# Performance work log

Measured on AMD Instinct MI355X. Metric: run time of the kernel, lower is better.

## Reference

```python
import jax, jax.numpy as jnp
import numpy as np

N = 50000      # nodes in the graph (len(vertices))
E = 800000     # edges per adjacency
D = 128        # n_feature (pretrained embedding dim)
V = 100000     # n_input (entity vocab)
OUT = 20       # n_output
L = 7          # n_hidden layers
BN_EPS = 1e-5


def setup_inputs() -> dict:
    key = jax.random.key(0)
    ks = jax.random.split(key, 12)
    s = 1.0 / np.sqrt(D)
    return {
        "vertices": jax.random.randint(ks[0], (N,), 0, V),
        "edge_index": jax.random.randint(ks[1], (L, 2, E), 0, N),
        "edge_weight": jax.random.uniform(ks[2], (L, E), jnp.float32),
        "emb_table": jax.random.normal(ks[3], (V, D), jnp.float32) * 0.02,
        "gcn_w_hidden": jax.random.normal(ks[4], (L - 1, D, D), jnp.float32) * s,
        "gcn_b_hidden": jnp.zeros((L - 1, D), jnp.float32),
        "gcn_w_out": jax.random.normal(ks[5], (D, OUT), jnp.float32) * s,
        "gcn_b_out": jnp.zeros((OUT,), jnp.float32),
        "bn_gamma_hidden": jnp.ones((L - 1, D), jnp.float32),
        "bn_beta_hidden": jnp.zeros((L - 1, D), jnp.float32),
        "bn_gamma_out": jnp.ones((OUT,), jnp.float32),
        "bn_beta_out": jnp.zeros((OUT,), jnp.float32),
        "te_wl": jax.random.normal(ks[6], (L - 1, D, D), jnp.float32) * s,
        "te_wc": jax.random.normal(ks[7], (L - 1, D, D), jnp.float32) * s,
        "te_b": jnp.zeros((L - 1, D), jnp.float32),
        "mask_w": jax.random.normal(ks[8], (V,), jnp.float32) * 0.02,
        "mask_b": jnp.zeros((OUT,), jnp.float32),
    }


def _spmm(src, dst, w, x):
    # out[i] = sum_{e: dst[e]==i} w[e] * x[src[e]]  (sparse adj @ x)
    return jax.ops.segment_sum(w[:, None] * x[src], dst, num_segments=N)


def _batchnorm(x, gamma, beta):
    # BatchNorm1d over the node (batch) axis, training-mode batch statistics
    m = x.mean(axis=0)
    v = x.var(axis=0)
    return (x - m) * jax.lax.rsqrt(v + BN_EPS) * gamma + beta


def reference(vertices, edge_index, edge_weight, emb_table,
              gcn_w_hidden, gcn_b_hidden, gcn_w_out, gcn_b_out,
              bn_gamma_hidden, bn_beta_hidden, bn_gamma_out, bn_beta_out,
              te_wl, te_wc, te_b, mask_w, mask_b):
    x = emb_table[vertices]                               # [N, D]
    for i in range(L):
        last_x = x
        if i < L - 1:
            support = x @ gcn_w_hidden[i]                 # [N, D]
            h = _spmm(edge_index[i, 0], edge_index[i, 1], edge_weight[i], support)
            h = h + gcn_b_hidden[i]
            h = _batchnorm(h, bn_gamma_hidden[i], bn_beta_hidden[i])
            h = jax.nn.relu(h)                            # dropout: eval mode (identity)
            j = (i - 1) % (L - 1)  # faithful to temporal_cells[i-1] (i=0 hits index -1)
            g = jax.nn.sigmoid(last_x @ te_wl[j] + h @ te_wc[j] + te_b[j])
            x = g * h + (1.0 - g) * last_x                # temporal gating cell
        else:
            support = x @ gcn_w_out                       # [N, OUT]
            h = _spmm(edge_index[i, 0], edge_index[i, 1], edge_weight[i], support)
            h = h + gcn_b_out
            x = _batchnorm(h, bn_gamma_out, bn_beta_out)
    x = jax.nn.relu(x)                                    # [N, OUT]
    out = jax.nn.sigmoid(mask_w[vertices] @ x + mask_b)   # MaskLinear + sigmoid -> [OUT]
    return out
```

## Files before the change

### kernel.cpp

```cpp
#include <hip/hip_runtime.h>
#include <hip/hip_fp16.h>

#define NN 50000
#define EE 800000
#define DIM 128
#define OUTC 20
#define LL 7
#define LE (LL*EE)
#define LN (LL*NN)
#define BN_EPS 1e-5f
#define LSTRIDE 136
#define NREP 64
#define NBUK 196
#define GMS  200
#define NBLK 200
#define CH   4000
#define CH4  (CH/4)
#define SCN  (LL*NBUK*NBLK)
#define FSCAP 4864
#define STATSZ (6*NREP*256 + 8*64 + 8*32 + 8)
#define STATSZ4 (STATSZ/4)

typedef __attribute__((ext_vector_type(8))) short short8;
typedef __attribute__((ext_vector_type(4))) float f32x4;

static __device__ __forceinline__ float sigm(float z){ return 1.0f/(1.0f+expf(-z)); }
static __device__ __forceinline__ unsigned short f2bf(float f){
  unsigned int u = __float_as_uint(f);
  u += 0x7FFF + ((u>>16)&1);
  return (unsigned short)(u>>16);
}
static __device__ __forceinline__ float bf2f(unsigned short s){
  return __uint_as_float(((unsigned int)s)<<16);
}

__global__ __launch_bounds__(256) void k_pre(const float* __restrict__ wh,
    const float* __restrict__ tewl, const float* __restrict__ tewc,
    const float* __restrict__ wout,
    unsigned short* __restrict__ Wt, unsigned short* __restrict__ WtO,
    const int* __restrict__ ei, int* __restrict__ Gm, float* __restrict__ stats){
  int bid = blockIdx.x;
  int t = threadIdx.x;
  if (bid < 1152){
    int gid = bid*256+t;
    int m = gid>>14; int idx = gid&16383;
    int n = idx>>7, k = idx&127;
    const float* src = (m<6)? wh + (size_t)m*16384
                     : (m<12)? tewl + (size_t)(m-6)*16384
                     : tewc + (size_t)(m-12)*16384;
    Wt[gid] = f2bf(src[k*128+n]);
  } else if (bid < 1168){
    int idx = (bid-1152)*256+t;
    int n = idx>>7, k = idx&127;
    WtO[idx] = (n<OUTC)? f2bf(wout[k*OUTC+n]) : (unsigned short)0;
  } else if (bid < 2568){
    int bb = bid-1168;
    int l = bb / NBLK, b = bb - l*NBLK;
    __shared__ int h[NBUK];
    if (t<NBUK) h[t]=0;
    const int4* dsts = (const int4*)(ei + (size_t)(2*l+1)*EE + b*CH);
    int4 dv[4];
    #pragma unroll
    for (int i=0;i<4;i++){
      int k4 = t + i*256;
      if (k4<CH4) dv[i] = dsts[k4];
    }
    __syncthreads();
    #pragma unroll
    for (int i=0;i<4;i++){
      int k4 = t + i*256;
      if (k4<CH4){
        atomicAdd(&h[dv[i].x>>8], 1);
        atomicAdd(&h[dv[i].y>>8], 1);
        atomicAdd(&h[dv[i].z>>8], 1);
        atomicAdd(&h[dv[i].w>>8], 1);
      }
    }
    __syncthreads();
    int* g = Gm + (size_t)(l*NBLK+b)*GMS;
    if (t<NBUK) g[t]=h[t];
  } else {
    int z = (bid-2568)*256+t;
    if (z < STATSZ4) ((float4*)stats)[z] = make_float4(0.f,0.f,0.f,0.f);
  }
}

__global__ __launch_bounds__(256) void k_scan1p(const int* __restrict__ Gm,
    int* __restrict__ part, int* __restrict__ bsums){
  __shared__ int s[256];
  int t = threadIdx.x;
  int base = blockIdx.x*4096 + t*16;
  int v[16]; int sum = 0;
  #pragma unroll
  for (int i=0;i<16;i++){
    int idx = base+i; int val = 0;
    if (idx < SCN){
      int l = idx/(NBUK*NBLK);
      int r = idx - l*(NBUK*NBLK);
      int buk = r/NBLK, b = r - buk*NBLK;
      val = Gm[(size_t)(l*NBLK+b)*GMS + buk];
    }
    v[i]=val; sum+=val;
  }
  s[t]=sum; __syncthreads();
  for (int off=1; off<256; off<<=1){
    int x = (t>=off)? s[t-off] : 0;
    __syncthreads(); s[t]+=x; __syncthreads();
  }
  if (t==255) bsums[blockIdx.x] = s[255];
  int run = s[t]-sum;
  #pragma unroll
  for (int i=0;i<16;i++){ if (base+i<SCN) part[base+i]=run; run += v[i]; }
}

__global__ __launch_bounds__(1024) void k_scan2(int* bsums, int nb){
  __shared__ int s[1024];
  int t=threadIdx.x;
  int v = (t<nb)? bsums[t]:0;
  s[t]=v; __syncthreads();
  for (int off=1; off<1024; off<<=1){
    int x=(t>=off)? s[t-off]:0; __syncthreads(); s[t]+=x; __syncthreads();
  }
  if (t<nb) bsums[t] = s[t]-v;
}

__global__ __launch_bounds__(256) void k_bscatter(const int* __restrict__ ei,
    const float* __restrict__ ew, const int* __restrict__ S,
    const int* __restrict__ bsums, const int* __restrict__ Gm,
    unsigned int* __restrict__ btmpP, unsigned char* __restrict__ btmpD){
  int l = blockIdx.x / NBLK, b = blockIdx.x - l*NBLK;
  int t = threadIdx.x;
  __shared__ int bstart[NBUK], cur[NBUK], runb[NBUK];
  __shared__ int wsum[4];
  __shared__ unsigned int  ebP[CH];
  __shared__ unsigned short ebM[CH];
  const int4*   srcs = (const int4*)(ei + (size_t)(2*l)*EE + b*CH);
  const int4*   dsts = (const int4*)(ei + (size_t)(2*l+1)*EE + b*CH);
  const float4* wsrc = (const float4*)(ew + (size_t)l*EE + b*CH);
  int4 sv[4], dv[4]; float4 wv[4];
  #pragma unroll
  for (int i=0;i<4;i++){
    int k4 = t + i*256;
    if (k4<CH4){
      sv[i] = srcs[k4];
      dv[i] = dsts[k4];
      wv[i] = wsrc[k4];
    }
  }
  int v = (t<NBUK)? Gm[(size_t)(l*NBLK+b)*GMS + t] : 0;
  int incl = v;
  #pragma unroll
  for (int d=1; d<64; d<<=1){
    int n = __shfl_up(incl, d, 64);
    if ((t&63) >= d) incl += n;
  }
  if ((t&63)==63) wsum[t>>6] = incl;
  __syncthreads();
  {
    int wv_ = t>>6, add = 0;
    if (wv_>0) add += wsum[0];
    if (wv_>1) add += wsum[1];
    if (wv_>2) add += wsum[2];
    incl += add;
  }
  if (t<NBUK){
    bstart[t]=incl-v; cur[t]=incl-v;
    int sidx = (l*NBUK+t)*NBLK + b;
    runb[t] = S[sidx] + bsums[sidx>>12];
  }
  __syncthreads();
  #define PUTE(SRC,DST,WF) { int buk=(DST)>>8; int pos=atomicAdd(&cur[buk],1); \
    unsigned short hw=__half_as_ushort(__float2half(WF)); \
    ebP[pos]=(unsigned)(SRC)|((unsigned)hw<<16); \
    ebM[pos]=(unsigned short)(((DST)&255)|(buk<<8)); }
  #pragma unroll
  for (int i=0;i<4;i++){
    int k4 = t + i*256;
    if (k4<CH4){
      PUTE(sv[i].x, dv[i].x, wv[i].x);
      PUTE(sv[i].y, dv[i].y, wv[i].y);
      PUTE(sv[i].z, dv[i].z, wv[i].z);
      PUTE(sv[i].w, dv[i].w, wv[i].w);
    }
  }
  #undef PUTE
  __syncthreads();
  for (int k=t;k<CH;k+=256){
    unsigned short m = ebM[k];
    int buk = m>>8;
    int gp = runb[buk] + (k - bstart[buk]);
    btmpP[gp] = ebP[k];
    btmpD[gp] = (unsigned char)(m&255);
  }
}

__global__ __launch_bounds__(256) void k_fsort(const unsigned int* __restrict__ btmpP,
    const unsigned char* __restrict__ btmpD, const int* __restrict__ S,
    const int* __restrict__ bsums,
    unsigned int* __restrict__ sedge, int* __restrict__ offs){
  int lbuk = blockIdx.x;
  int l = lbuk/NBUK, bl = lbuk - l*NBUK;
  int t = threadIdx.x;
  int i0 = lbuk*NBLK, i1 = i0+NBLK;
  int base = S[i0] + bsums[i0>>12];
  int end  = (i1==SCN)? LE : (S[i1] + bsums[i1>>12]);
  int nE = end - base;
  __shared__ int cnt[256];
  __shared__ int wsum[4];
  __shared__ unsigned int stg[FSCAP];
  cnt[t]=0;
  __syncthreads();
  for (int k=t; k<nE; k+=256) atomicAdd(&cnt[btmpD[base+k]], 1);
  __syncthreads();
  int c = cnt[t];
  int incl = c;
  #pragma unroll
  for (int d=1; d<64; d<<=1){
    int n = __shfl_up(incl, d, 64);
    if ((t&63) >= d) incl += n;
  }
  if ((t&63)==63) wsum[t>>6] = incl;
  __syncthreads();
  {
    int wv_ = t>>6, add = 0;
    if (wv_>0) add += wsum[0];
    if (wv_>1) add += wsum[1];
    if (wv_>2) add += wsum[2];
    incl += add;
  }
  int excl = incl - c;
  {
    int node = bl*256+t;
    if (node<NN) offs[(size_t)l*NN+node] = base + excl;
  }
  if (lbuk==0 && t==255) offs[LN]=LE;
  if (nE <= FSCAP){
    cnt[t] = excl;
    __syncthreads();
    for (int k=t; k<nE; k+=256){
      int d = btmpD[base+k];
      int r = atomicAdd(&cnt[d],1);
      stg[r] = btmpP[base+k];
    }
    __syncthreads();
    for (int k=t; k<nE; k+=256) sedge[base+k] = stg[k];
  } else {
    cnt[t] = base + excl;
    __syncthreads();
    for (int k=t; k<nE; k+=256){
      int d = btmpD[base+k];
      int r = atomicAdd(&cnt[d],1);
      sedge[r] = btmpP[base+k];
    }
  }
}

__global__ __launch_bounds__(256) void k_gemm_sup_emb(const int* __restrict__ verts,
    const float* __restrict__ emb, const unsigned short* __restrict__ Wt,
    unsigned short* __restrict__ Y, unsigned short* __restrict__ xout, int M){
  __shared__ unsigned short Xs[32*LSTRIDE];
  int tid = threadIdx.x;
  int row0 = blockIdx.x*32;
  #pragma unroll
  for (int it=0; it<2; it++){
    int idx = tid + it*256;
    int r = idx>>4, k8 = idx&15;
    short8 w = short8(0);
    if (row0+r < M){
      int v = verts[row0+r];
      const float4* p = (const float4*)emb + (size_t)v*32 + k8*2;
      float4 v0 = p[0], v1 = p[1];
      w[0]=(short)f2bf(v0.x); w[1]=(short)f2bf(v0.y); w[2]=(short)f2bf(v0.z); w[3]=(short)f2bf(v0.w);
      w[4]=(short)f2bf(v1.x); w[5]=(short)f2bf(v1.y); w[6]=(short)f2bf(v1.z); w[7]=(short)f2bf(v1.w);
      *(short8*)(xout + (size_t)(row0+r)*128 + k8*8) = w;
    }
    *(short8*)&Xs[r*LSTRIDE + k8*8] = w;
  }
  __syncthreads();
  int w = tid>>6, lane = tid&63, m = lane&15, q = lane>>4;
  int rw = (w&1)*16, cw = (w>>1)*64;
  f32x4 acc[4];
  #pragma unroll
  for (int nt=0;nt<4;nt++){ acc[nt][0]=0.f; acc[nt][1]=0.f; acc[nt][2]=0.f; acc[nt][3]=0.f; }
  #pragma unroll
  for (int kc=0; kc<4; kc++){
    short8 a = *(const short8*)&Xs[(rw+m)*LSTRIDE + kc*32 + 8*q];
    #pragma unroll
    for (int nt=0; nt<4; nt++){
      short8 b = *(const short8*)&Wt[(size_t)(cw+nt*16+m)*128 + kc*32 + 8*q];
      acc[nt] = __builtin_amdgcn_mfma_f32_16x16x32_bf16(a, b, acc[nt], 0,0,0);
    }
  }
  #pragma unroll
  for (int nt=0; nt<4; nt++){
    #pragma unroll
    for (int i=0;i<4;i++){
      int rr = row0 + rw + 4*q + i;
      if (rr<M) Y[(size_t)rr*128 + cw + nt*16 + m] = f2bf(acc[nt][i]);
    }
  }
}

template<int FUSE>
__global__ __launch_bounds__(256,4) void k_gemm_gate2(const unsigned short* __restrict__ H,
    const float* __restrict__ stL,
    const float* __restrict__ gamma, const float* __restrict__ beta,
    const unsigned short* __restrict__ Wl, const unsigned short* __restrict__ Wc,
    const unsigned short* __restrict__ Wn, const float* __restrict__ teb,
    unsigned short* __restrict__ x, unsigned short* __restrict__ supY, int M){
  __shared__ unsigned short XsX[64*LSTRIDE];
  __shared__ unsigned short XsH[64*LSTRIDE];
  __shared__ float sSt[256];
  int tid = threadIdx.x;
  int row0 = blockIdx.x*64;
  int k8 = tid&15;
  int w = tid>>6, lane = tid&63, m = lane&15, q = lane>>4;
  int cw = w*32;
  float4 g0 = *(const float4*)(gamma + k8*8), g1 = *(const float4*)(gamma + k8*8 + 4);
  float4 b0v = *(const float4*)(beta  + k8*8), b1v = *(const float4*)(beta  + k8*8 + 4);
  float tb0 = teb[cw+m], tb1 = teb[cw+16+m];
  short8 xv[4], hv[4];
  #pragma unroll
  for (int it=0; it<4; it++){
    int r = (tid + it*256)>>4;
    xv[it] = short8(0); hv[it] = short8(0);
    if (row0+r < M){
      xv[it] = *(const short8*)(x + (size_t)(row0+r)*128 + k8*8);
      hv[it] = *(const short8*)(H + (size_t)(row0+r)*128 + k8*8);
    }
  }
  {
    float sacc = 0.f;
    #pragma unroll 8
    for (int g=0; g<NREP; g++) sacc += stL[g*256 + tid];
    sSt[tid] = sacc;
  }
  #pragma unroll
  for (int it=0; it<4; it++){
    int r = (tid + it*256)>>4;
    *(short8*)&XsX[r*LSTRIDE + k8*8] = xv[it];
  }
  __syncthreads();
  float scv[8], ofv[8];
  {
    const float gam[8] = {g0.x,g0.y,g0.z,g0.w,g1.x,g1.y,g1.z,g1.w};
    const float bet[8] = {b0v.x,b0v.y,b0v.z,b0v.w,b1v.x,b1v.y,b1v.z,b1v.w};
    #pragma unroll
    for (int j=0;j<8;j++){
      float s  = sSt[k8*8+j];
      float sq = sSt[128 + k8*8+j];
      float mean = s*(1.0f/NN);
      float var  = sq*(1.0f/NN) - mean*mean;
      float r = rsqrtf(var+BN_EPS)*gam[j];
      scv[j]=r; ofv[j]=bet[j]-mean*r;
    }
  }
  #pragma unroll
  for (int it=0; it<4; it++){
    int r = (tid + it*256)>>4;
    short8 wv_;
    #pragma unroll
    for (int j=0;j<8;j++){
      float o = bf2f((unsigned short)hv[it][j]);
      wv_[j] = (short)f2bf(fmaxf(fmaf(o, scv[j], ofv[j]), 0.f));
    }
    *(short8*)&XsH[r*LSTRIDE + k8*8] = wv_;
  }
  __syncthreads();
  f32x4 acc[4][2];
  #pragma unroll
  for (int rt=0;rt<4;rt++)
    #pragma unroll
    for (int nt=0;nt<2;nt++){ acc[rt][nt][0]=0.f; acc[rt][nt][1]=0.f; acc[rt][nt][2]=0.f; acc[rt][nt][3]=0.f; }
  #pragma unroll
  for (int kc=0; kc<4; kc++){
    short8 b0 = *(const short8*)&Wl[(size_t)(cw+m)*128 + kc*32 + 8*q];
    short8 b1 = *(const short8*)&Wl[(size_t)(cw+16+m)*128 + kc*32 + 8*q];
    #pragma unroll
    for (int rt=0; rt<4; rt++){
      short8 a = *(const short8*)&XsX[(rt*16+m)*LSTRIDE + kc*32 + 8*q];
      acc[rt][0] = __builtin_amdgcn_mfma_f32_16x16x32_bf16(a, b0, acc[rt][0], 0,0,0);
      acc[rt][1] = __builtin_amdgcn_mfma_f32_16x16x32_bf16(a, b1, acc[rt][1], 0,0,0);
    }
  }
  #pragma unroll
  for (int kc=0; kc<4; kc++){
    short8 b0 = *(const short8*)&Wc[(size_t)(cw+m)*128 + kc*32 + 8*q];
    short8 b1 = *(const short8*)&Wc[(size_t)(cw+16+m)*128 + kc*32 + 8*q];
    #pragma unroll
    for (int rt=0; rt<4; rt++){
      short8 a = *(const short8*)&XsH[(rt*16+m)*LSTRIDE + kc*32 + 8*q];
      acc[rt][0] = __builtin_amdgcn_mfma_f32_16x16x32_bf16(a, b0, acc[rt][0], 0,0,0);
      acc[rt][1] = __builtin_amdgcn_mfma_f32_16x16x32_bf16(a, b1, acc[rt][1], 0,0,0);
    }
  }
  __syncthreads();
  #pragma unroll
  for (int rt=0; rt<4; rt++){
    #pragma unroll
    for (int nt=0; nt<2; nt++){
      int col = cw + nt*16 + m;
      float bias = nt? tb1 : tb0;
      #pragma unroll
      for (int i=0;i<4;i++){
        int lr = rt*16 + 4*q + i;
        float hvv = bf2f(XsH[lr*LSTRIDE + col]);
        float xo  = bf2f(XsX[lr*LSTRIDE + col]);
        float g = sigm(acc[rt][nt][i] + bias);
        unsigned short xnb = f2bf(g*hvv + (1.f-g)*xo);
        XsH[lr*LSTRIDE + col] = xnb;
        if (FUSE==1) XsX[lr*LSTRIDE + col] = xnb;
      }
    }
  }
  __syncthreads();
  #pragma unroll
  for (int it=0; it<4; it++){
    int r = (tid + it*256)>>4;
    if (row0+r < M)
      *(short8*)(x + (size_t)(row0+r)*128 + k8*8) = *(short8*)&XsH[r*LSTRIDE + k8*8];
  }
  if (FUSE==1){
    #pragma unroll
    for (int rt=0;rt<4;rt++)
      #pragma unroll
      for (int nt=0;nt<2;nt++){ acc[rt][nt][0]=0.f; acc[rt][nt][1]=0.f; acc[rt][nt][2]=0.f; acc[rt][nt][3]=0.f; }
    #pragma unroll
    for (int kc=0; kc<4; kc++){
      short8 b0 = *(const short8*)&Wn[(size_t)(cw+m)*128 + kc*32 + 8*q];
      short8 b1 = *(const short8*)&Wn[(size_t)(cw+16+m)*128 + kc*32 + 8*q];
      #pragma unroll
      for (int rt=0; rt<4; rt++){
        short8 a = *(const short8*)&XsX[(rt*16+m)*LSTRIDE + kc*32 + 8*q];
        acc[rt][0] = __builtin_amdgcn_mfma_f32_16x16x32_bf16(a, b0, acc[rt][0], 0,0,0);
        acc[rt][1] = __builtin_amdgcn_mfma_f32_16x16x32_bf16(a, b1, acc[rt][1], 0,0,0);
      }
    }
    #pragma unroll
    for (int rt=0; rt<4; rt++){
      #pragma unroll
      for (int nt=0; nt<2; nt++){
        #pragma unroll
        for (int i=0;i<4;i++){
          int rr = row0 + rt*16 + 4*q + i;
          if (rr<M) supY[(size_t)rr*128 + cw + nt*16 + m] = f2bf(acc[rt][nt][i]);
        }
      }
    }
  }
  if (FUSE==2){
    if (w < 2){
      f32x4 ao[2][2];
      #pragma unroll
      for (int rt=0;rt<2;rt++)
        #pragma unroll
        for (int nt=0;nt<2;nt++){ ao[rt][nt][0]=0.f; ao[rt][nt][1]=0.f; ao[rt][nt][2]=0.f; ao[rt][nt][3]=0.f; }
      #pragma unroll
      for (int kc=0; kc<4; kc++){
        short8 b0 = *(const short8*)&Wn[(size_t)(m)*128 + kc*32 + 8*q];
        short8 b1 = *(const short8*)&Wn[(size_t)(16+m)*128 + kc*32 + 8*q];
        #pragma unroll
        for (int rt=0; rt<2; rt++){
          short8 a = *(const short8*)&XsH[((w*2+rt)*16+m)*LSTRIDE + kc*32 + 8*q];
          ao[rt][0] = __builtin_amdgcn_mfma_f32_16x16x32_bf16(a, b0, ao[rt][0], 0,0,0);
          ao[rt][1] = __builtin_amdgcn_mfma_f32_16x16x32_bf16(a, b1, ao[rt][1], 0,0,0);
        }
      }
      #pragma unroll
      for (int rt=0; rt<2; rt++){
        #pragma unroll
        for (int nt=0; nt<2; nt++){
          #pragma unroll
          for (int i=0;i<4;i++){
            int rr = row0 + (w*2+rt)*16 + 4*q + i;
            if (rr<M) supY[(size_t)rr*32 + nt*16 + m] = f2bf(ao[rt][nt][i]);
          }
        }
      }
    }
  }
}

__global__ __launch_bounds__(256) void k_spmm128(const unsigned short* __restrict__ sup,
    const unsigned int* __restrict__ sedge, const int* __restrict__ offs,
    unsigned short* __restrict__ h, int lbase, float* __restrict__ stL){
  int nl = threadIdx.x>>5;
  int node = blockIdx.x*8 + nl;
  int fq = threadIdx.x & 31;
  int p = offs[lbase+node], end = offs[lbase+node+1];
  float4 a0 = make_float4(0.f,0.f,0.f,0.f), a1 = a0, a2 = a0, a3 = a0;
  for (; p+7<end; p+=8){
    unsigned int ev[8];
    #pragma unroll
    for (int u=0;u<8;u++) ev[u] = __builtin_nontemporal_load(sedge+p+u);
    ushort4 sv[8];
    #pragma unroll
    for (int u=0;u<8;u++) sv[u] = *(const ushort4*)(sup + (size_t)(ev[u]&0xFFFFu)*128 + fq*4);
    #pragma unroll
    for (int u=0;u<8;u++){
      float w = __half2float(__ushort_as_half((unsigned short)(ev[u]>>16)));
      float4& a = (u&3)==0? a0 : (u&3)==1? a1 : (u&3)==2? a2 : a3;
      a.x += w*bf2f(sv[u].x); a.y += w*bf2f(sv[u].y);
      a.z += w*bf2f(sv[u].z); a.w += w*bf2f(sv[u].w);
    }
  }
  for (; p+3<end; p+=4){
    unsigned int e0 = __builtin_nontemporal_load(sedge+p);
    unsigned int e1 = __builtin_nontemporal_load(sedge+p+1);
    unsigned int e2 = __builtin_nontemporal_load(sedge+p+2);
    unsigned int e3 = __builtin_nontemporal_load(sedge+p+3);
    ushort4 s0 = *(const ushort4*)(sup + (size_t)(e0&0xFFFFu)*128 + fq*4);
    ushort4 s1 = *(const ushort4*)(sup + (size_t)(e1&0xFFFFu)*128 + fq*4);
    ushort4 s2 = *(const ushort4*)(sup + (size_t)(e2&0xFFFFu)*128 + fq*4);
    ushort4 s3 = *(const ushort4*)(sup + (size_t)(e3&0xFFFFu)*128 + fq*4);
    float w0 = __half2float(__ushort_as_half((unsigned short)(e0>>16)));
    float w1 = __half2float(__ushort_as_half((unsigned short)(e1>>16)));
    float w2 = __half2float(__ushort_as_half((unsigned short)(e2>>16)));
    float w3 = __half2float(__ushort_as_half((unsigned short)(e3>>16)));
    a0.x += w0*bf2f(s0.x); a0.y += w0*bf2f(s0.y); a0.z += w0*bf2f(s0.z); a0.w += w0*bf2f(s0.w);
    a1.x += w1*bf2f(s1.x); a1.y += w1*bf2f(s1.y); a1.z += w1*bf2f(s1.z); a1.w += w1*bf2f(s1.w);
    a2.x += w2*bf2f(s2.x); a2.y += w2*bf2f(s2.y); a2.z += w2*bf2f(s2.z); a2.w += w2*bf2f(s2.w);
    a3.x += w3*bf2f(s3.x); a3.y += w3*bf2f(s3.y); a3.z += w3*bf2f(s3.z); a3.w += w3*bf2f(s3.w);
  }
  for (; p<end; p++){
    unsigned int e0 = __builtin_nontemporal_load(sedge+p);
    float w0 = __half2float(__ushort_as_half((unsigned short)(e0>>16)));
    ushort4 s0 = *(const ushort4*)(sup + (size_t)(e0&0xFFFFu)*128 + fq*4);
    a0.x += w0*bf2f(s0.x); a0.y += w0*bf2f(s0.y); a0.z += w0*bf2f(s0.z); a0.w += w0*bf2f(s0.w);
  }
  a0.x+=a1.x+a2.x+a3.x; a0.y+=a1.y+a2.y+a3.y;
  a0.z+=a1.z+a2.z+a3.z; a0.w+=a1.w+a2.w+a3.w;
  ushort4 ov;
  ov.x=f2bf(a0.x); ov.y=f2bf(a0.y); ov.z=f2bf(a0.z); ov.w=f2bf(a0.w);
  *(ushort4*)(h + (size_t)node*128 + fq*4) = ov;
  __shared__ float sP[8][132], sQ[8][132];
  int f0 = fq*4;
  sP[nl][f0+0]=a0.x; sP[nl][f0+1]=a0.y; sP[nl][f0+2]=a0.z; sP[nl][f0+3]=a0.w;
  sQ[nl][f0+0]=a0.x*a0.x; sQ[nl][f0+1]=a0.y*a0.y; sQ[nl][f0+2]=a0.z*a0.z; sQ[nl][f0+3]=a0.w*a0.w;
  __syncthreads();
  if (threadIdx.x < 128){
    int f = threadIdx.x;
    float s=0.f, sq=0.f;
    #pragma unroll
    for (int n=0;n<8;n++){ s += sP[n][f]; sq += sQ[n][f]; }
    float* base = stL + (blockIdx.x & (NREP-1))*256;
    atomicAdd(&base[f], s); atomicAdd(&base[128+f], sq);
  }
}

__global__ __launch_bounds__(256) void k_spmm_out(const unsigned short* __restrict__ sup,
    const unsigned int* __restrict__ sedge, const int* __restrict__ offs,
    float* __restrict__ h, int lbase, float* __restrict__ st8){
  int nl = threadIdx.x>>5;
  int node = blockIdx.x*8 + nl;
  int c = threadIdx.x & 31;
  bool act = c < OUTC;
  int p = offs[lbase+node], end = offs[lbase+node+1];
  float a0=0.f,a1=0.f,a2=0.f,a3=0.f;
  for (; p+7<end; p+=8){
    unsigned int ev[8];
    #pragma unroll
    for (int u=0;u<8;u++) ev[u] = __builtin_nontemporal_load(sedge+p+u);
    float sv[8];
    #pragma unroll
    for (int u=0;u<8;u++) sv[u] = bf2f(sup[(size_t)(ev[u]&0xFFFFu)*32 + c]);
    #pragma unroll
    for (int u=0;u<8;u++){
      float w = __half2float(__ushort_as_half((unsigned short)(ev[u]>>16)));
      if ((u&3)==0) a0 += w*sv[u];
      else if ((u&3)==1) a1 += w*sv[u];
      else if ((u&3)==2) a2 += w*sv[u];
      else a3 += w*sv[u];
    }
  }
  for (; p<end; p++){
    unsigned int e = __builtin_nontemporal_load(sedge+p);
    float w = __half2float(__ushort_as_half((unsigned short)(e>>16)));
    a0 += w*bf2f(sup[(size_t)(e&0xFFFFu)*32 + c]);
  }
  float v = a0+a1+a2+a3;
  if (act) h[(size_t)node*OUTC+c] = v;
  if (!act) v = 0.f;
  __shared__ float sS[8][33], sQ[8][33];
  sS[nl][c] = v; sQ[nl][c] = v*v;
  __syncthreads();
  if (threadIdx.x < 32){
    float s=0.f, sq=0.f;
    #pragma unroll
    for (int n=0;n<8;n++){ s += sS[n][c]; sq += sQ[n][c]; }
    if (c<OUTC){
      float* base = st8 + (blockIdx.x&7)*64;
      atomicAdd(&base[c], s); atomicAdd(&base[32+c], sq);
    }
  }
}

__global__ __launch_bounds__(256) void k_reduce(const float* __restrict__ xf,
    const float* __restrict__ st8, const float* __restrict__ gamma,
    const float* __restrict__ beta, const int* __restrict__ verts,
    const float* __restrict__ mw, float* __restrict__ acc8, int rpb,
    const float* __restrict__ mb, float* __restrict__ outp, int* __restrict__ tick,
    int nblocks){
  int c = threadIdx.x & 31, g = threadIdx.x >> 5;
  float scn=0.f, offc=0.f;
  if (c<OUTC){
    float s=0.f, sq=0.f;
    #pragma unroll
    for (int i=0;i<8;i++){ s += st8[i*64+c]; sq += st8[i*64+32+c]; }
    const float invN = 1.0f/NN;
    float m = s*invN;
    float var = sq*invN - m*m;
    scn = rsqrtf(var+BN_EPS)*gamma[c];
    offc = beta[c] - m*scn;
  }
  int r0 = blockIdx.x*rpb;
  int r1 = min(NN, r0+rpb);
  float s=0.f;
  for (int r=r0+g; r<r1; r+=8){
    float m = mw[verts[r]];
    if (c<OUTC){
      float v = fmaxf(fmaf(xf[(size_t)r*OUTC+c], scn, offc), 0.f);
      s += m * v;
    }
  }
  __shared__ float sh[256];
  sh[threadIdx.x]=s; __syncthreads();
  if (threadIdx.x<32){
    #pragma unroll
    for (int i=1;i<8;i++) s += sh[threadIdx.x + i*32];
    if (c<OUTC) atomicAdd(&acc8[(blockIdx.x&7)*32 + c], s);
  }
  __syncthreads();
  __shared__ int lastf;
  if (threadIdx.x==0){
    __threadfence();
    int tk = __hip_atomic_fetch_add(tick, 1, __ATOMIC_ACQ_REL, __HIP_MEMORY_SCOPE_AGENT);
    lastf = (tk == nblocks-1);
  }
  __syncthreads();
  if (lastf && threadIdx.x < 32 && c < OUTC){
    float s2=0.f;
    #pragma unroll
    for (int gg=0; gg<8; gg++)
      s2 += __hip_atomic_load(&acc8[gg*32+c], __ATOMIC_RELAXED, __HIP_MEMORY_SCOPE_AGENT);
    outp[c] = sigm(s2+mb[c]);
  }
}

extern "C" void kernel_launch(void* const* d_in, const int* in_sizes, int n_in,
                              void* d_out, int out_size, void* d_ws, size_t ws_size,
                              hipStream_t stream){
  const int*   verts = (const int*)d_in[0];
  const int*   ei    = (const int*)d_in[1];
  const float* ew    = (const float*)d_in[2];
  const float* emb   = (const float*)d_in[3];
  const float* wh    = (const float*)d_in[4];
  const float* w_out = (const float*)d_in[6];
  const float* bng_h = (const float*)d_in[8];
  const float* bnb_h = (const float*)d_in[9];
  const float* bng_o = (const float*)d_in[10];
  const float* bnb_o = (const float*)d_in[11];
  const float* tewl  = (const float*)d_in[12];
  const float* tewc  = (const float*)d_in[13];
  const float* teb   = (const float*)d_in[14];
  const float* maskw = (const float*)d_in[15];
  const float* maskb = (const float*)d_in[16];
  float* out = (float*)d_out;

  char* ws = (char*)d_ws;
  size_t off=0;
  auto alloc=[&](size_t bytes)->char*{ char* p = ws+off; off += (bytes+255)&~(size_t)255; return p; };
  unsigned int* sedge = (unsigned int*)alloc(sizeof(int)*LE);
  int*   offs   = (int*)  alloc(sizeof(int)*(LN+1));
  int*   Gm     = (int*)  alloc(sizeof(int)*LL*NBLK*GMS);
  int*   S      = (int*)  alloc(sizeof(int)*(SCN+1));
  int*   bsums  = (int*)  alloc(sizeof(int)*1024);
  unsigned short* xbf   = (unsigned short*)alloc(sizeof(short)*NN*DIM);
  unsigned short* supbf = (unsigned short*)alloc(sizeof(short)*NN*DIM);
  unsigned short* hbf   = (unsigned short*)alloc(sizeof(short)*NN*DIM);
  unsigned short* supO  = (unsigned short*)alloc(sizeof(short)*NN*32);
  unsigned short* Wt = (unsigned short*)alloc(sizeof(short)*18*DIM*DIM);
  unsigned short* WtO = (unsigned short*)alloc(sizeof(short)*32*DIM);
  float* stats  = (float*)alloc(sizeof(float)*STATSZ);
  float* ostat8 = stats + 6*NREP*256;
  float* racc8  = ostat8 + 8*64;
  int*   tick   = (int*)(racc8 + 8*32);
  unsigned int*  btmpP = (unsigned int*)xbf;
  unsigned char* btmpD = (unsigned char*)hbf;

  k_pre<<<2665,256,0,stream>>>(wh, tewl, tewc, w_out, Wt, WtO, ei, Gm, stats);
  int nsb = (SCN+4095)/4096;
  k_scan1p<<<nsb,256,0,stream>>>(Gm, S, bsums);
  k_scan2<<<1,1024,0,stream>>>(bsums, nsb);
  k_bscatter<<<LL*NBLK,256,0,stream>>>(ei, ew, S, bsums, Gm, btmpP, btmpD);
  k_fsort<<<LL*NBUK,256,0,stream>>>(btmpP, btmpD, S, bsums, sedge, offs);

  k_gemm_sup_emb<<<(NN+31)/32,256,0,stream>>>(verts, emb, Wt, supbf, xbf, NN);
  for (int i=0;i<6;i++){
    int j = (i==0)?5:(i-1);
    float* stL = stats + i*NREP*256;
    k_spmm128<<<NN/8,256,0,stream>>>(supbf, sedge, offs, hbf, i*NN, stL);
    if (i<5)
      k_gemm_gate2<1><<<(NN+63)/64,256,0,stream>>>(hbf, stL,
          bng_h+(size_t)i*DIM, bnb_h+(size_t)i*DIM,
          Wt + (size_t)(6+j)*DIM*DIM, Wt + (size_t)(12+j)*DIM*DIM,
          Wt + (size_t)(i+1)*DIM*DIM, teb + (size_t)j*DIM, xbf, supbf, NN);
    else
      k_gemm_gate2<2><<<(NN+63)/64,256,0,stream>>>(hbf, stL,
          bng_h+(size_t)i*DIM, bnb_h+(size_t)i*DIM,
          Wt + (size_t)(6+j)*DIM*DIM, Wt + (size_t)(12+j)*DIM*DIM,
          WtO, teb + (size_t)j*DIM, xbf, supO, NN);
  }

  k_spmm_out<<<NN/8,256,0,stream>>>(supO, sedge, offs, (float*)hbf, 6*NN, ostat8);
  float* bufO = (float*)hbf;
  k_reduce<<<512,256,0,stream>>>(bufO, ostat8, bng_o, bnb_o, verts, maskw, racc8, 98,
                                 maskb, out, tick, 512);
}
```

Baseline: 655.5 us.

## Merge GCN layer kernels into one persistent cooperative kernel with grid syncs

Replaces the sequence of per-layer kernels (embedding GEMM, six SpMM plus gate-GEMM pairs, output SpMM and final reduce) with one persistent cooperative kernel. Blocks grid-stride over tiles and separate the phases with grid.sync(). The aim is to remove the launch overhead and inter-kernel gaps of roughly fifteen launches. The cost is that a grid-wide barrier now sits between phases, the grid is capped at occupancy times 256 CUs, and the larger fused kernel shares one register budget, which can lower occupancy.

New measurement: 1.980 ms. 3.02x slower.

```diff
diff --git a/kernel.cpp b/kernel.cpp
--- a/kernel.cpp
+++ b/kernel.cpp
@@ -1,5 +1,8 @@
 #include <hip/hip_runtime.h>
 #include <hip/hip_fp16.h>
+#include <hip/hip_cooperative_groups.h>
+
+namespace cg = cooperative_groups;
 
 #define NN 50000
 #define EE 800000
@@ -255,395 +258,398 @@
   }
 }
 
-__global__ __launch_bounds__(256) void k_gemm_sup_emb(const int* __restrict__ verts,
-    const float* __restrict__ emb, const unsigned short* __restrict__ Wt,
-    unsigned short* __restrict__ Y, unsigned short* __restrict__ xout, int M){
-  __shared__ unsigned short Xs[32*LSTRIDE];
-  int tid = threadIdx.x;
-  int row0 = blockIdx.x*32;
-  #pragma unroll
-  for (int it=0; it<2; it++){
-    int idx = tid + it*256;
-    int r = idx>>4, k8 = idx&15;
-    short8 w = short8(0);
-    if (row0+r < M){
-      int v = verts[row0+r];
-      const float4* p = (const float4*)emb + (size_t)v*32 + k8*2;
-      float4 v0 = p[0], v1 = p[1];
-      w[0]=(short)f2bf(v0.x); w[1]=(short)f2bf(v0.y); w[2]=(short)f2bf(v0.z); w[3]=(short)f2bf(v0.w);
-      w[4]=(short)f2bf(v1.x); w[5]=(short)f2bf(v1.y); w[6]=(short)f2bf(v1.z); w[7]=(short)f2bf(v1.w);
-      *(short8*)(xout + (size_t)(row0+r)*128 + k8*8) = w;
-    }
-    *(short8*)&Xs[r*LSTRIDE + k8*8] = w;
-  }
-  __syncthreads();
-  int w = tid>>6, lane = tid&63, m = lane&15, q = lane>>4;
-  int rw = (w&1)*16, cw = (w>>1)*64;
-  f32x4 acc[4];
-  #pragma unroll
-  for (int nt=0;nt<4;nt++){ acc[nt][0]=0.f; acc[nt][1]=0.f; acc[nt][2]=0.f; acc[nt][3]=0.f; }
-  #pragma unroll
-  for (int kc=0; kc<4; kc++){
-    short8 a = *(const short8*)&Xs[(rw+m)*LSTRIDE + kc*32 + 8*q];
-    #pragma unroll
-    for (int nt=0; nt<4; nt++){
-      short8 b = *(const short8*)&Wt[(size_t)(cw+nt*16+m)*128 + kc*32 + 8*q];
-      acc[nt] = __builtin_amdgcn_mfma_f32_16x16x32_bf16(a, b, acc[nt], 0,0,0);
-    }
-  }
-  #pragma unroll
-  for (int nt=0; nt<4; nt++){
-    #pragma unroll
-    for (int i=0;i<4;i++){
-      int rr = row0 + rw + 4*q + i;
-      if (rr<M) Y[(size_t)rr*128 + cw + nt*16 + m] = f2bf(acc[nt][i]);
-    }
-  }
-}
-
-template<int FUSE>
-__global__ __launch_bounds__(256,4) void k_gemm_gate2(const unsigned short* __restrict__ H,
-    const float* __restrict__ stL,
-    const float* __restrict__ gamma, const float* __restrict__ beta,
-    const unsigned short* __restrict__ Wl, const unsigned short* __restrict__ Wc,
-    const unsigned short* __restrict__ Wn, const float* __restrict__ teb,
-    unsigned short* __restrict__ x, unsigned short* __restrict__ supY, int M){
+struct KP {
+  const int* verts; const float* emb;
+  const unsigned short* Wt; const unsigned short* WtO;
+  const unsigned int* sedge; const int* offs;
+  unsigned short* xbf; unsigned short* supbf; unsigned short* hbf; unsigned short* supO;
+  float* stats; float* ostat8; float* racc8;
+  const float* bng_h; const float* bnb_h; const float* bng_o; const float* bnb_o;
+  const float* teb; const float* maskw; const float* maskb; float* out;
+};
+
+__global__ __launch_bounds__(256,4) void k_net(KP p){
   __shared__ unsigned short XsX[64*LSTRIDE];
   __shared__ unsigned short XsH[64*LSTRIDE];
   __shared__ float sSt[256];
-  int tid = threadIdx.x;
-  int row0 = blockIdx.x*64;
-  int k8 = tid&15;
-  int w = tid>>6, lane = tid&63, m = lane&15, q = lane>>4;
-  int cw = w*32;
-  float4 g0 = *(const float4*)(gamma + k8*8), g1 = *(const float4*)(gamma + k8*8 + 4);
-  float4 b0v = *(const float4*)(beta  + k8*8), b1v = *(const float4*)(beta  + k8*8 + 4);
-  float tb0 = teb[cw+m], tb1 = teb[cw+16+m];
-  short8 xv[4], hv[4];
-  #pragma unroll
-  for (int it=0; it<4; it++){
-    int r = (tid + it*256)>>4;
-    xv[it] = short8(0); hv[it] = short8(0);
-    if (row0+r < M){
-      xv[it] = *(const short8*)(x + (size_t)(row0+r)*128 + k8*8);
-      hv[it] = *(const short8*)(H + (size_t)(row0+r)*128 + k8*8);
-    }
-  }
-  {
-    float sacc = 0.f;
-    #pragma unroll 8
-    for (int g=0; g<NREP; g++) sacc += stL[g*256 + tid];
-    sSt[tid] = sacc;
-  }
-  #pragma unroll
-  for (int it=0; it<4; it++){
-    int r = (tid + it*256)>>4;
-    *(short8*)&XsX[r*LSTRIDE + k8*8] = xv[it];
-  }
-  __syncthreads();
-  float scv[8], ofv[8];
-  {
-    const float gam[8] = {g0.x,g0.y,g0.z,g0.w,g1.x,g1.y,g1.z,g1.w};
-    const float bet[8] = {b0v.x,b0v.y,b0v.z,b0v.w,b1v.x,b1v.y,b1v.z,b1v.w};
+  cg::grid_group grid = cg::this_grid();
+  const int nb = gridDim.x;
+  const int tid = threadIdx.x;
+  const int k8 = tid&15;
+  const int w = tid>>6, lane = tid&63, m = lane&15, q = lane>>4;
+
+  for (int tile = blockIdx.x; tile < (NN+31)/32; tile += nb){
+    int row0 = tile*32;
     #pragma unroll
-    for (int j=0;j<8;j++){
-      float s  = sSt[k8*8+j];
-      float sq = sSt[128 + k8*8+j];
-      float mean = s*(1.0f/NN);
-      float var  = sq*(1.0f/NN) - mean*mean;
-      float r = rsqrtf(var+BN_EPS)*gam[j];
-      scv[j]=r; ofv[j]=bet[j]-mean*r;
-    }
-  }
-  #pragma unroll
-  for (int it=0; it<4; it++){
-    int r = (tid + it*256)>>4;
-    short8 wv_;
+    for (int it=0; it<2; it++){
+      int idx = tid + it*256;
+      int r = idx>>4, kk = idx&15;
+      short8 wv_ = short8(0);
+      if (row0+r < NN){
+        int v = p.verts[row0+r];
+        const float4* pp = (const float4*)p.emb + (size_t)v*32 + kk*2;
+        float4 v0 = pp[0], v1 = pp[1];
+        wv_[0]=(short)f2bf(v0.x); wv_[1]=(short)f2bf(v0.y); wv_[2]=(short)f2bf(v0.z); wv_[3]=(short)f2bf(v0.w);
+        wv_[4]=(short)f2bf(v1.x); wv_[5]=(short)f2bf(v1.y); wv_[6]=(short)f2bf(v1.z); wv_[7]=(short)f2bf(v1.w);
+        *(short8*)(p.xbf + (size_t)(row0+r)*128 + kk*8) = wv_;
+      }
+      *(short8*)&XsX[r*LSTRIDE + kk*8] = wv_;
+    }
+    __syncthreads();
+    int rw = (w&1)*16, cw = (w>>1)*64;
+    f32x4 acc[4];
     #pragma unroll
-    for (int j=0;j<8;j++){
-      float o = bf2f((unsigned short)hv[it][j]);
-      wv_[j] = (short)f2bf(fmaxf(fmaf(o, scv[j], ofv[j]), 0.f));
-    }
-    *(short8*)&XsH[r*LSTRIDE + k8*8] = wv_;
-  }
-  __syncthreads();
-  f32x4 acc[4][2];
-  #pragma unroll
-  for (int rt=0;rt<4;rt++)
+    for (int nt=0;nt<4;nt++){ acc[nt][0]=0.f; acc[nt][1]=0.f; acc[nt][2]=0.f; acc[nt][3]=0.f; }
     #pragma unroll
-    for (int nt=0;nt<2;nt++){ acc[rt][nt][0]=0.f; acc[rt][nt][1]=0.f; acc[rt][nt][2]=0.f; acc[rt][nt][3]=0.f; }
-  #pragma unroll
-  for (int kc=0; kc<4; kc++){
-    short8 b0 = *(const short8*)&Wl[(size_t)(cw+m)*128 + kc*32 + 8*q];
-    short8 b1 = *(const short8*)&Wl[(size_t)(cw+16+m)*128 + kc*32 + 8*q];
+    for (int kc=0; kc<4; kc++){
+      short8 a = *(const short8*)&XsX[(rw+m)*LSTRIDE + kc*32 + 8*q];
+      #pragma unroll
+      for (int nt=0; nt<4; nt++){
+        short8 b = *(const short8*)&p.Wt[(size_t)(cw+nt*16+m)*128 + kc*32 + 8*q];
+        acc[nt] = __builtin_amdgcn_mfma_f32_16x16x32_bf16(a, b, acc[nt], 0,0,0);
+      }
+    }
     #pragma unroll
-    for (int rt=0; rt<4; rt++){
-      short8 a = *(const short8*)&XsX[(rt*16+m)*LSTRIDE + kc*32 + 8*q];
-      acc[rt][0] = __builtin_amdgcn_mfma_f32_16x16x32_bf16(a, b0, acc[rt][0], 0,0,0);
-      acc[rt][1] = __builtin_amdgcn_mfma_f32_16x16x32_bf16(a, b1, acc[rt][1], 0,0,0);
-    }
-  }
-  #pragma unroll
-  for (int kc=0; kc<4; kc++){
-    short8 b0 = *(const short8*)&Wc[(size_t)(cw+m)*128 + kc*32 + 8*q];
-    short8 b1 = *(const short8*)&Wc[(size_t)(cw+16+m)*128 + kc*32 + 8*q];
-    #pragma unroll
-    for (int rt=0; rt<4; rt++){
-      short8 a = *(const short8*)&XsH[(rt*16+m)*LSTRIDE + kc*32 + 8*q];
-      acc[rt][0] = __builtin_amdgcn_mfma_f32_16x16x32_bf16(a, b0, acc[rt][0], 0,0,0);
-      acc[rt][1] = __builtin_amdgcn_mfma_f32_16x16x32_bf16(a, b1, acc[rt][1], 0,0,0);
-    }
-  }
-  __syncthreads();
-  #pragma unroll
-  for (int rt=0; rt<4; rt++){
-    #pragma unroll
-    for (int nt=0; nt<2; nt++){
-      int col = cw + nt*16 + m;
-      float bias = nt? tb1 : tb0;
+    for (int nt=0; nt<4; nt++){
       #pragma unroll
       for (int i=0;i<4;i++){
-        int lr = rt*16 + 4*q + i;
-        float hvv = bf2f(XsH[lr*LSTRIDE + col]);
-        float xo  = bf2f(XsX[lr*LSTRIDE + col]);
-        float g = sigm(acc[rt][nt][i] + bias);
-        unsigned short xnb = f2bf(g*hvv + (1.f-g)*xo);
-        XsH[lr*LSTRIDE + col] = xnb;
-        if (FUSE==1) XsX[lr*LSTRIDE + col] = xnb;
-      }
-    }
-  }
-  __syncthreads();
-  #pragma unroll
-  for (int it=0; it<4; it++){
-    int r = (tid + it*256)>>4;
-    if (row0+r < M)
-      *(short8*)(x + (size_t)(row0+r)*128 + k8*8) = *(short8*)&XsH[r*LSTRIDE + k8*8];
-  }
-  if (FUSE==1){
+        int rr = row0 + rw + 4*q + i;
+        if (rr<NN) p.supbf[(size_t)rr*128 + cw + nt*16 + m] = f2bf(acc[nt][i]);
+      }
+    }
+    __syncthreads();
+  }
+  grid.sync();
+
+  for (int L=0; L<6; L++){
+    const int fuse = (L<5);
+    const int j = (L==0)?5:(L-1);
+    float* stL = p.stats + (size_t)L*NREP*256;
+    const unsigned short* Wl = p.Wt + (size_t)(6+j)*DIM*DIM;
+    const unsigned short* Wc = p.Wt + (size_t)(12+j)*DIM*DIM;
+    const unsigned short* Wn = fuse? (p.Wt + (size_t)(L+1)*DIM*DIM) : p.WtO;
+    const float* gamma = p.bng_h + (size_t)L*DIM;
+    const float* beta  = p.bnb_h + (size_t)L*DIM;
+    const float* tebL  = p.teb + (size_t)j*DIM;
+    const int lbase = L*NN;
+
+    {
+      float* sP = (float*)XsX;
+      float* sQ = sP + 8*132;
+      int nl = tid>>5;
+      int fq = tid & 31;
+      for (int gix = blockIdx.x; gix < NN/8; gix += nb){
+        int node = gix*8 + nl;
+        int pp = p.offs[lbase+node], end = p.offs[lbase+node+1];
+        float4 a0 = make_float4(0.f,0.f,0.f,0.f), a1 = a0, a2 = a0, a3 = a0;
+        for (; pp+7<end; pp+=8){
+          unsigned int ev[8];
+          #pragma unroll
+          for (int u=0;u<8;u++) ev[u] = __builtin_nontemporal_load(p.sedge+pp+u);
+          ushort4 sv[8];
+          #pragma unroll
+          for (int u=0;u<8;u++) sv[u] = *(const ushort4*)(p.supbf + (size_t)(ev[u]&0xFFFFu)*128 + fq*4);
+          #pragma unroll
+          for (int u=0;u<8;u++){
+            float ww = __half2float(__ushort_as_half((unsigned short)(ev[u]>>16)));
+            float4& a = (u&3)==0? a0 : (u&3)==1? a1 : (u&3)==2? a2 : a3;
+            a.x += ww*bf2f(sv[u].x); a.y += ww*bf2f(sv[u].y);
+            a.z += ww*bf2f(sv[u].z); a.w += ww*bf2f(sv[u].w);
+          }
+        }
+        for (; pp<end; pp++){
+          unsigned int e0 = __builtin_nontemporal_load(p.sedge+pp);
+          float w0 = __half2float(__ushort_as_half((unsigned short)(e0>>16)));
+          ushort4 s0 = *(const ushort4*)(p.supbf + (size_t)(e0&0xFFFFu)*128 + fq*4);
+          a0.x += w0*bf2f(s0.x); a0.y += w0*bf2f(s0.y); a0.z += w0*bf2f(s0.z); a0.w += w0*bf2f(s0.w);
+        }
+        a0.x+=a1.x+a2.x+a3.x; a0.y+=a1.y+a2.y+a3.y;
+        a0.z+=a1.z+a2.z+a3.z; a0.w+=a1.w+a2.w+a3.w;
+        ushort4 ov;
+        ov.x=f2bf(a0.x); ov.y=f2bf(a0.y); ov.z=f2bf(a0.z); ov.w=f2bf(a0.w);
+        *(ushort4*)(p.hbf + (size_t)node*128 + fq*4) = ov;
+        int f0 = fq*4;
+        sP[nl*132+f0+0]=a0.x; sP[nl*132+f0+1]=a0.y; sP[nl*132+f0+2]=a0.z; sP[nl*132+f0+3]=a0.w;
+        sQ[nl*132+f0+0]=a0.x*a0.x; sQ[nl*132+f0+1]=a0.y*a0.y; sQ[nl*132+f0+2]=a0.z*a0.z; sQ[nl*132+f0+3]=a0.w*a0.w;
+        __syncthreads();
+        if (tid < 128){
+          int f = tid;
+          float s=0.f, sq=0.f;
+          #pragma unroll
+          for (int n=0;n<8;n++){ s += sP[n*132+f]; sq += sQ[n*132+f]; }
+          float* base = stL + (gix & (NREP-1))*256;
+          atomicAdd(&base[f], s); atomicAdd(&base[128+f], sq);
+        }
+        __syncthreads();
+      }
+    }
+    grid.sync();
+
+    {
+      int cw = w*32;
+      unsigned short* supY = fuse? p.supbf : p.supO;
+      for (int tile = blockIdx.x; tile < (NN+63)/64; tile += nb){
+        int row0 = tile*64;
+        float4 g0 = *(const float4*)(gamma + k8*8), g1 = *(const float4*)(gamma + k8*8 + 4);
+        float4 b0v = *(const float4*)(beta  + k8*8), b1v = *(const float4*)(beta  + k8*8 + 4);
+        float tb0 = tebL[cw+m], tb1 = tebL[cw+16+m];
+        short8 xv[4], hv[4];
+        #pragma unroll
+        for (int it=0; it<4; it++){
+          int r = (tid + it*256)>>4;
+          xv[it] = short8(0); hv[it] = short8(0);
+          if (row0+r < NN){
+            xv[it] = *(const short8*)(p.xbf + (size_t)(row0+r)*128 + k8*8);
+            hv[it] = *(const short8*)(p.hbf + (size_t)(row0+r)*128 + k8*8);
+          }
+        }
+        {
+          float sacc = 0.f;
+          #pragma unroll 8
+          for (int g=0; g<NREP; g++) sacc += stL[g*256 + tid];
+          sSt[tid] = sacc;
+        }
+        #pragma unroll
+        for (int it=0; it<4; it++){
+          int r = (tid + it*256)>>4;
+          *(short8*)&XsX[r*LSTRIDE + k8*8] = xv[it];
+        }
+        __syncthreads();
+        float scv[8], ofv[8];
+        {
+          const float gam[8] = {g0.x,g0.y,g0.z,g0.w,g1.x,g1.y,g1.z,g1.w};
+          const float bet[8] = {b0v.x,b0v.y,b0v.z,b0v.w,b1v.x,b1v.y,b1v.z,b1v.w};
+          #pragma unroll
+          for (int jj=0;jj<8;jj++){
+            float s  = sSt[k8*8+jj];
+            float sq = sSt[128 + k8*8+jj];
+            float mean = s*(1.0f/NN);
+            float var  = sq*(1.0f/NN) - mean*mean;
+            float r = rsqrtf(var+BN_EPS)*gam[jj];
+            scv[jj]=r; ofv[jj]=bet[jj]-mean*r;
+          }
+        }
+        #pragma unroll
+        for (int it=0; it<4; it++){
+          int r = (tid + it*256)>>4;
+          short8 wv_;
+          #pragma unroll
+          for (int jj=0;jj<8;jj++){
+            float o = bf2f((unsigned short)hv[it][jj]);
+            wv_[jj] = (short)f2bf(fmaxf(fmaf(o, scv[jj], ofv[jj]), 0.f));
+          }
+          *(short8*)&XsH[r*LSTRIDE + k8*8] = wv_;
+        }
+        __syncthreads();
+        f32x4 acc[4][2];
+        #pragma unroll
+        for (int rt=0;rt<4;rt++)
+          #pragma unroll
+          for (int nt=0;nt<2;nt++){ acc[rt][nt][0]=0.f; acc[rt][nt][1]=0.f; acc[rt][nt][2]=0.f; acc[rt][nt][3]=0.f; }
+        #pragma unroll
+        for (int kc=0; kc<4; kc++){
+          short8 b0 = *(const short8*)&Wl[(size_t)(cw+m)*128 + kc*32 + 8*q];
+          short8 b1 = *(const short8*)&Wl[(size_t)(cw+16+m)*128 + kc*32 + 8*q];
+          #pragma unroll
+          for (int rt=0; rt<4; rt++){
+            short8 a = *(const short8*)&XsX[(rt*16+m)*LSTRIDE + kc*32 + 8*q];
+            acc[rt][0] = __builtin_amdgcn_mfma_f32_16x16x32_bf16(a, b0, acc[rt][0], 0,0,0);
+            acc[rt][1] = __builtin_amdgcn_mfma_f32_16x16x32_bf16(a, b1, acc[rt][1], 0,0,0);
+          }
+        }
+        #pragma unroll
+        for (int kc=0; kc<4; kc++){
+          short8 b0 = *(const short8*)&Wc[(size_t)(cw+m)*128 + kc*32 + 8*q];
+          short8 b1 = *(const short8*)&Wc[(size_t)(cw+16+m)*128 + kc*32 + 8*q];
+          #pragma unroll
+          for (int rt=0; rt<4; rt++){
+            short8 a = *(const short8*)&XsH[(rt*16+m)*LSTRIDE + kc*32 + 8*q];
+            acc[rt][0] = __builtin_amdgcn_mfma_f32_16x16x32_bf16(a, b0, acc[rt][0], 0,0,0);
+            acc[rt][1] = __builtin_amdgcn_mfma_f32_16x16x32_bf16(a, b1, acc[rt][1], 0,0,0);
+          }
+        }
+        __syncthreads();
+        #pragma unroll
+        for (int rt=0; rt<4; rt++){
+          #pragma unroll
+          for (int nt=0; nt<2; nt++){
+            int col = cw + nt*16 + m;
+            float bias = nt? tb1 : tb0;
+            #pragma unroll
+            for (int i=0;i<4;i++){
+              int lr = rt*16 + 4*q + i;
+              float hvv = bf2f(XsH[lr*LSTRIDE + col]);
+              float xo  = bf2f(XsX[lr*LSTRIDE + col]);
+              float g = sigm(acc[rt][nt][i] + bias);
+              unsigned short xnb = f2bf(g*hvv + (1.f-g)*xo);
+              XsH[lr*LSTRIDE + col] = xnb;
+              if (fuse) XsX[lr*LSTRIDE + col] = xnb;
+            }
+          }
+        }
+        __syncthreads();
+        #pragma unroll
+        for (int it=0; it<4; it++){
+          int r = (tid + it*256)>>4;
+          if (row0+r < NN)
+            *(short8*)(p.xbf + (size_t)(row0+r)*128 + k8*8) = *(short8*)&XsH[r*LSTRIDE + k8*8];
+        }
+        if (fuse){
+          #pragma unroll
+          for (int rt=0;rt<4;rt++)
+            #pragma unroll
+            for (int nt=0;nt<2;nt++){ acc[rt][nt][0]=0.f; acc[rt][nt][1]=0.f; acc[rt][nt][2]=0.f; acc[rt][nt][3]=0.f; }
+          #pragma unroll
+          for (int kc=0; kc<4; kc++){
+            short8 b0 = *(const short8*)&Wn[(size_t)(cw+m)*128 + kc*32 + 8*q];
+            short8 b1 = *(const short8*)&Wn[(size_t)(cw+16+m)*128 + kc*32 + 8*q];
+            #pragma unroll
+            for (int rt=0; rt<4; rt++){
+              short8 a = *(const short8*)&XsX[(rt*16+m)*LSTRIDE + kc*32 + 8*q];
+              acc[rt][0] = __builtin_amdgcn_mfma_f32_16x16x32_bf16(a, b0, acc[rt][0], 0,0,0);
+              acc[rt][1] = __builtin_amdgcn_mfma_f32_16x16x32_bf16(a, b1, acc[rt][1], 0,0,0);
+            }
+          }
+          #pragma unroll
+          for (int rt=0; rt<4; rt++){
+            #pragma unroll
+            for (int nt=0; nt<2; nt++){
+              #pragma unroll
+              for (int i=0;i<4;i++){
+                int rr = row0 + rt*16 + 4*q + i;
+                if (rr<NN) supY[(size_t)rr*128 + cw + nt*16 + m] = f2bf(acc[rt][nt][i]);
+              }
+            }
+          }
+        } else {
+          if (w < 2){
+            f32x4 ao[2][2];
+            #pragma unroll
+            for (int rt=0;rt<2;rt++)
+              #pragma unroll
+              for (int nt=0;nt<2;nt++){ ao[rt][nt][0]=0.f; ao[rt][nt][1]=0.f; ao[rt][nt][2]=0.f; ao[rt][nt][3]=0.f; }
+            #pragma unroll
+            for (int kc=0; kc<4; kc++){
+              short8 b0 = *(const short8*)&Wn[(size_t)(m)*128 + kc*32 + 8*q];
+              short8 b1 = *(const short8*)&Wn[(size_t)(16+m)*128 + kc*32 + 8*q];
+              #pragma unroll
+              for (int rt=0; rt<2; rt++){
+                short8 a = *(const short8*)&XsH[((w*2+rt)*16+m)*LSTRIDE + kc*32 + 8*q];
+                ao[rt][0] = __builtin_amdgcn_mfma_f32_16x16x32_bf16(a, b0, ao[rt][0], 0,0,0);
+                ao[rt][1] = __builtin_amdgcn_mfma_f32_16x16x32_bf16(a, b1, ao[rt][1], 0,0,0);
+              }
+            }
+            #pragma unroll
+            for (int rt=0; rt<2; rt++){
+              #pragma unroll
+              for (int nt=0; nt<2; nt++){
+                #pragma unroll
+                for (int i=0;i<4;i++){
+                  int rr = row0 + (w*2+rt)*16 + 4*q + i;
+                  if (rr<NN) supY[(size_t)rr*32 + nt*16 + m] = f2bf(ao[rt][nt][i]);
+                }
+              }
+            }
+          }
+        }
+        __syncthreads();
+      }
+    }
+    grid.sync();
+  }
+
+  {
+    float* sS = (float*)XsX;
+    float* sQ2 = sS + 8*33;
+    int nl = tid>>5;
+    int c = tid & 31;
+    bool act = c < OUTC;
+    float* hout = (float*)p.hbf;
+    for (int gix = blockIdx.x; gix < NN/8; gix += nb){
+      int node = gix*8 + nl;
+      int pp = p.offs[6*NN+node], end = p.offs[6*NN+node+1];
+      float a0=0.f,a1=0.f,a2=0.f,a3=0.f;
+      for (; pp+7<end; pp+=8){
+        unsigned int ev[8];
+        #pragma unroll
+        for (int u=0;u<8;u++) ev[u] = __builtin_nontemporal_load(p.sedge+pp+u);
+        float sv[8];
+        #pragma unroll
+        for (int u=0;u<8;u++) sv[u] = bf2f(p.supO[(size_t)(ev[u]&0xFFFFu)*32 + c]);
+        #pragma unroll
+        for (int u=0;u<8;u++){
+          float ww = __half2float(__ushort_as_half((unsigned short)(ev[u]>>16)));
+          if ((u&3)==0) a0 += ww*sv[u];
+          else if ((u&3)==1) a1 += ww*sv[u];
+          else if ((u&3)==2) a2 += ww*sv[u];
+          else a3 += ww*sv[u];
+        }
+      }
+      for (; pp<end; pp++){
+        unsigned int e = __builtin_nontemporal_load(p.sedge+pp);
+        float ww = __half2float(__ushort_as_half((unsigned short)(e>>16)));
+        a0 += ww*bf2f(p.supO[(size_t)(e&0xFFFFu)*32 + c]);
+      }
+      float v = a0+a1+a2+a3;
+      if (act) hout[(size_t)node*OUTC+c] = v;
+      if (!act) v = 0.f;
+      sS[nl*33+c] = v; sQ2[nl*33+c] = v*v;
+      __syncthreads();
+      if (tid < 32){
+        float s=0.f, sq=0.f;
+        #pragma unroll
+        for (int n=0;n<8;n++){ s += sS[n*33+c]; sq += sQ2[n*33+c]; }
+        if (c<OUTC){
+          float* base = p.ostat8 + (gix&7)*64;
+          atomicAdd(&base[c], s); atomicAdd(&base[32+c], sq);
+        }
+      }
+      __syncthreads();
+    }
+  }
+  grid.sync();
+
+  {
+    int c = tid & 31, g = tid >> 5;
+    const float* hout = (const float*)p.hbf;
+    float scn=0.f, offc=0.f;
+    if (c<OUTC){
+      float s=0.f, sq=0.f;
+      #pragma unroll
+      for (int i=0;i<8;i++){ s += p.ostat8[i*64+c]; sq += p.ostat8[i*64+32+c]; }
+      const float invN = 1.0f/NN;
+      float mn = s*invN;
+      float var = sq*invN - mn*mn;
+      scn = rsqrtf(var+BN_EPS)*p.bng_o[c];
+      offc = p.bnb_o[c] - mn*scn;
+    }
+    for (int slice = blockIdx.x; slice < 512; slice += nb){
+      int r0 = slice*98;
+      int r1 = min(NN, r0+98);
+      float s=0.f;
+      for (int r=r0+g; r<r1; r+=8){
+        float mm = p.maskw[p.verts[r]];
+        if (c<OUTC){
+          float v = fmaxf(fmaf(hout[(size_t)r*OUTC+c], scn, offc), 0.f);
+          s += mm * v;
+        }
+      }
+      sSt[tid]=s; __syncthreads();
+      if (tid<32){
+        #pragma unroll
+        for (int i=1;i<8;i++) s += sSt[tid + i*32];
+        if (c<OUTC) atomicAdd(&p.racc8[(slice&7)*32 + c], s);
+      }
+      __syncthreads();
+    }
+  }
+  grid.sync();
+
+  if (blockIdx.x==0 && tid<OUTC){
+    float s=0.f;
     #pragma unroll
-    for (int rt=0;rt<4;rt++)
-      #pragma unroll
-      for (int nt=0;nt<2;nt++){ acc[rt][nt][0]=0.f; acc[rt][nt][1]=0.f; acc[rt][nt][2]=0.f; acc[rt][nt][3]=0.f; }
-    #pragma unroll
-    for (int kc=0; kc<4; kc++){
-      short8 b0 = *(const short8*)&Wn[(size_t)(cw+m)*128 + kc*32 + 8*q];
-      short8 b1 = *(const short8*)&Wn[(size_t)(cw+16+m)*128 + kc*32 + 8*q];
-      #pragma unroll
-      for (int rt=0; rt<4; rt++){
-        short8 a = *(const short8*)&XsX[(rt*16+m)*LSTRIDE + kc*32 + 8*q];
-        acc[rt][0] = __builtin_amdgcn_mfma_f32_16x16x32_bf16(a, b0, acc[rt][0], 0,0,0);
-        acc[rt][1] = __builtin_amdgcn_mfma_f32_16x16x32_bf16(a, b1, acc[rt][1], 0,0,0);
-      }
-    }
-    #pragma unroll
-    for (int rt=0; rt<4; rt++){
-      #pragma unroll
-      for (int nt=0; nt<2; nt++){
-        #pragma unroll
-        for (int i=0;i<4;i++){
-          int rr = row0 + rt*16 + 4*q + i;
-          if (rr<M) supY[(size_t)rr*128 + cw + nt*16 + m] = f2bf(acc[rt][nt][i]);
-        }
-      }
-    }
-  }
-  if (FUSE==2){
-    if (w < 2){
-      f32x4 ao[2][2];
-      #pragma unroll
-      for (int rt=0;rt<2;rt++)
-        #pragma unroll
-        for (int nt=0;nt<2;nt++){ ao[rt][nt][0]=0.f; ao[rt][nt][1]=0.f; ao[rt][nt][2]=0.f; ao[rt][nt][3]=0.f; }
-      #pragma unroll
-      for (int kc=0; kc<4; kc++){
-        short8 b0 = *(const short8*)&Wn[(size_t)(m)*128 + kc*32 + 8*q];
-        short8 b1 = *(const short8*)&Wn[(size_t)(16+m)*128 + kc*32 + 8*q];
-        #pragma unroll
-        for (int rt=0; rt<2; rt++){
-          short8 a = *(const short8*)&XsH[((w*2+rt)*16+m)*LSTRIDE + kc*32 + 8*q];
-          ao[rt][0] = __builtin_amdgcn_mfma_f32_16x16x32_bf16(a, b0, ao[rt][0], 0,0,0);
-          ao[rt][1] = __builtin_amdgcn_mfma_f32_16x16x32_bf16(a, b1, ao[rt][1], 0,0,0);
-        }
-      }
-      #pragma unroll
-      for (int rt=0; rt<2; rt++){
-        #pragma unroll
-        for (int nt=0; nt<2; nt++){
-          #pragma unroll
-          for (int i=0;i<4;i++){
-            int rr = row0 + (w*2+rt)*16 + 4*q + i;
-            if (rr<M) supY[(size_t)rr*32 + nt*16 + m] = f2bf(ao[rt][nt][i]);
-          }
-        }
-      }
-    }
-  }
-}
-
-__global__ __launch_bounds__(256) void k_spmm128(const unsigned short* __restrict__ sup,
-    const unsigned int* __restrict__ sedge, const int* __restrict__ offs,
-    unsigned short* __restrict__ h, int lbase, float* __restrict__ stL){
-  int nl = threadIdx.x>>5;
-  int node = blockIdx.x*8 + nl;
-  int fq = threadIdx.x & 31;
-  int p = offs[lbase+node], end = offs[lbase+node+1];
-  float4 a0 = make_float4(0.f,0.f,0.f,0.f), a1 = a0, a2 = a0, a3 = a0;
-  for (; p+7<end; p+=8){
-    unsigned int ev[8];
-    #pragma unroll
-    for (int u=0;u<8;u++) ev[u] = __builtin_nontemporal_load(sedge+p+u);
-    ushort4 sv[8];
-    #pragma unroll
-    for (int u=0;u<8;u++) sv[u] = *(const ushort4*)(sup + (size_t)(ev[u]&0xFFFFu)*128 + fq*4);
-    #pragma unroll
-    for (int u=0;u<8;u++){
-      float w = __half2float(__ushort_as_half((unsigned short)(ev[u]>>16)));
-      float4& a = (u&3)==0? a0 : (u&3)==1? a1 : (u&3)==2? a2 : a3;
-      a.x += w*bf2f(sv[u].x); a.y += w*bf2f(sv[u].y);
-      a.z += w*bf2f(sv[u].z); a.w += w*bf2f(sv[u].w);
-    }
-  }
-  for (; p+3<end; p+=4){
-    unsigned int e0 = __builtin_nontemporal_load(sedge+p);
-    unsigned int e1 = __builtin_nontemporal_load(sedge+p+1);
-    unsigned int e2 = __builtin_nontemporal_load(sedge+p+2);
-    unsigned int e3 = __builtin_nontemporal_load(sedge+p+3);
-    ushort4 s0 = *(const ushort4*)(sup + (size_t)(e0&0xFFFFu)*128 + fq*4);
-    ushort4 s1 = *(const ushort4*)(sup + (size_t)(e1&0xFFFFu)*128 + fq*4);
-    ushort4 s2 = *(const ushort4*)(sup + (size_t)(e2&0xFFFFu)*128 + fq*4);
-    ushort4 s3 = *(const ushort4*)(sup + (size_t)(e3&0xFFFFu)*128 + fq*4);
-    float w0 = __half2float(__ushort_as_half((unsigned short)(e0>>16)));
-    float w1 = __half2float(__ushort_as_half((unsigned short)(e1>>16)));
-    float w2 = __half2float(__ushort_as_half((unsigned short)(e2>>16)));
-    float w3 = __half2float(__ushort_as_half((unsigned short)(e3>>16)));
-    a0.x += w0*bf2f(s0.x); a0.y += w0*bf2f(s0.y); a0.z += w0*bf2f(s0.z); a0.w += w0*bf2f(s0.w);
-    a1.x += w1*bf2f(s1.x); a1.y += w1*bf2f(s1.y); a1.z += w1*bf2f(s1.z); a1.w += w1*bf2f(s1.w);
-    a2.x += w2*bf2f(s2.x); a2.y += w2*bf2f(s2.y); a2.z += w2*bf2f(s2.z); a2.w += w2*bf2f(s2.w);
-    a3.x += w3*bf2f(s3.x); a3.y += w3*bf2f(s3.y); a3.z += w3*bf2f(s3.z); a3.w += w3*bf2f(s3.w);
-  }
-  for (; p<end; p++){
-    unsigned int e0 = __builtin_nontemporal_load(sedge+p);
-    float w0 = __half2float(__ushort_as_half((unsigned short)(e0>>16)));
-    ushort4 s0 = *(const ushort4*)(sup + (size_t)(e0&0xFFFFu)*128 + fq*4);
-    a0.x += w0*bf2f(s0.x); a0.y += w0*bf2f(s0.y); a0.z += w0*bf2f(s0.z); a0.w += w0*bf2f(s0.w);
-  }
-  a0.x+=a1.x+a2.x+a3.x; a0.y+=a1.y+a2.y+a3.y;
-  a0.z+=a1.z+a2.z+a3.z; a0.w+=a1.w+a2.w+a3.w;
-  ushort4 ov;
-  ov.x=f2bf(a0.x); ov.y=f2bf(a0.y); ov.z=f2bf(a0.z); ov.w=f2bf(a0.w);
-  *(ushort4*)(h + (size_t)node*128 + fq*4) = ov;
-  __shared__ float sP[8][132], sQ[8][132];
-  int f0 = fq*4;
-  sP[nl][f0+0]=a0.x; sP[nl][f0+1]=a0.y; sP[nl][f0+2]=a0.z; sP[nl][f0+3]=a0.w;
-  sQ[nl][f0+0]=a0.x*a0.x; sQ[nl][f0+1]=a0.y*a0.y; sQ[nl][f0+2]=a0.z*a0.z; sQ[nl][f0+3]=a0.w*a0.w;
-  __syncthreads();
-  if (threadIdx.x < 128){
-    int f = threadIdx.x;
-    float s=0.f, sq=0.f;
-    #pragma unroll
-    for (int n=0;n<8;n++){ s += sP[n][f]; sq += sQ[n][f]; }
-    float* base = stL + (blockIdx.x & (NREP-1))*256;
-    atomicAdd(&base[f], s); atomicAdd(&base[128+f], sq);
-  }
-}
-
-__global__ __launch_bounds__(256) void k_spmm_out(const unsigned short* __restrict__ sup,
-    const unsigned int* __restrict__ sedge, const int* __restrict__ offs,
-    float* __restrict__ h, int lbase, float* __restrict__ st8){
-  int nl = threadIdx.x>>5;
-  int node = blockIdx.x*8 + nl;
-  int c = threadIdx.x & 31;
-  bool act = c < OUTC;
-  int p = offs[lbase+node], end = offs[lbase+node+1];
-  float a0=0.f,a1=0.f,a2=0.f,a3=0.f;
-  for (; p+7<end; p+=8){
-    unsigned int ev[8];
-    #pragma unroll
-    for (int u=0;u<8;u++) ev[u] = __builtin_nontemporal_load(sedge+p+u);
-    float sv[8];
-    #pragma unroll
-    for (int u=0;u<8;u++) sv[u] = bf2f(sup[(size_t)(ev[u]&0xFFFFu)*32 + c]);
-    #pragma unroll
-    for (int u=0;u<8;u++){
-      float w = __half2float(__ushort_as_half((unsigned short)(ev[u]>>16)));
-      if ((u&3)==0) a0 += w*sv[u];
-      else if ((u&3)==1) a1 += w*sv[u];
-      else if ((u&3)==2) a2 += w*sv[u];
-      else a3 += w*sv[u];
-    }
-  }
-  for (; p<end; p++){
-    unsigned int e = __builtin_nontemporal_load(sedge+p);
-    float w = __half2float(__ushort_as_half((unsigned short)(e>>16)));
-    a0 += w*bf2f(sup[(size_t)(e&0xFFFFu)*32 + c]);
-  }
-  float v = a0+a1+a2+a3;
-  if (act) h[(size_t)node*OUTC+c] = v;
-  if (!act) v = 0.f;
-  __shared__ float sS[8][33], sQ[8][33];
-  sS[nl][c] = v; sQ[nl][c] = v*v;
-  __syncthreads();
-  if (threadIdx.x < 32){
-    float s=0.f, sq=0.f;
-    #pragma unroll
-    for (int n=0;n<8;n++){ s += sS[n][c]; sq += sQ[n][c]; }
-    if (c<OUTC){
-      float* base = st8 + (blockIdx.x&7)*64;
-      atomicAdd(&base[c], s); atomicAdd(&base[32+c], sq);
-    }
-  }
-}
-
-__global__ __launch_bounds__(256) void k_reduce(const float* __restrict__ xf,
-    const float* __restrict__ st8, const float* __restrict__ gamma,
-    const float* __restrict__ beta, const int* __restrict__ verts,
-    const float* __restrict__ mw, float* __restrict__ acc8, int rpb,
-    const float* __restrict__ mb, float* __restrict__ outp, int* __restrict__ tick,
-    int nblocks){
-  int c = threadIdx.x & 31, g = threadIdx.x >> 5;
-  float scn=0.f, offc=0.f;
-  if (c<OUTC){
-    float s=0.f, sq=0.f;
-    #pragma unroll
-    for (int i=0;i<8;i++){ s += st8[i*64+c]; sq += st8[i*64+32+c]; }
-    const float invN = 1.0f/NN;
-    float m = s*invN;
-    float var = sq*invN - m*m;
-    scn = rsqrtf(var+BN_EPS)*gamma[c];
-    offc = beta[c] - m*scn;
-  }
-  int r0 = blockIdx.x*rpb;
-  int r1 = min(NN, r0+rpb);
-  float s=0.f;
-  for (int r=r0+g; r<r1; r+=8){
-    float m = mw[verts[r]];
-    if (c<OUTC){
-      float v = fmaxf(fmaf(xf[(size_t)r*OUTC+c], scn, offc), 0.f);
-      s += m * v;
-    }
-  }
-  __shared__ float sh[256];
-  sh[threadIdx.x]=s; __syncthreads();
-  if (threadIdx.x<32){
-    #pragma unroll
-    for (int i=1;i<8;i++) s += sh[threadIdx.x + i*32];
-    if (c<OUTC) atomicAdd(&acc8[(blockIdx.x&7)*32 + c], s);
-  }
-  __syncthreads();
-  __shared__ int lastf;
-  if (threadIdx.x==0){
-    __threadfence();
-    int tk = __hip_atomic_fetch_add(tick, 1, __ATOMIC_ACQ_REL, __HIP_MEMORY_SCOPE_AGENT);
-    lastf = (tk == nblocks-1);
-  }
-  __syncthreads();
-  if (lastf && threadIdx.x < 32 && c < OUTC){
-    float s2=0.f;
-    #pragma unroll
-    for (int gg=0; gg<8; gg++)
-      s2 += __hip_atomic_load(&acc8[gg*32+c], __ATOMIC_RELAXED, __HIP_MEMORY_SCOPE_AGENT);
-    outp[c] = sigm(s2+mb[c]);
+    for (int g=0; g<8; g++) s += p.racc8[g*32+tid];
+    p.out[tid] = sigm(s+p.maskb[tid]);
   }
 }
 
@@ -684,7 +690,6 @@
   float* stats  = (float*)alloc(sizeof(float)*STATSZ);
   float* ostat8 = stats + 6*NREP*256;
   float* racc8  = ostat8 + 8*64;
-  int*   tick   = (int*)(racc8 + 8*32);
   unsigned int*  btmpP = (unsigned int*)xbf;
   unsigned char* btmpD = (unsigned char*)hbf;
 
@@ -695,25 +700,21 @@
   k_bscatter<<<LL*NBLK,256,0,stream>>>(ei, ew, S, bsums, Gm, btmpP, btmpD);
   k_fsort<<<LL*NBUK,256,0,stream>>>(btmpP, btmpD, S, bsums, sedge, offs);
 
-  k_gemm_sup_emb<<<(NN+31)/32,256,0,stream>>>(verts, emb, Wt, supbf, xbf, NN);
-  for (int i=0;i<6;i++){
-    int j = (i==0)?5:(i-1);
-    float* stL = stats + i*NREP*256;
-    k_spmm128<<<NN/8,256,0,stream>>>(supbf, sedge, offs, hbf, i*NN, stL);
-    if (i<5)
-      k_gemm_gate2<1><<<(NN+63)/64,256,0,stream>>>(hbf, stL,
-          bng_h+(size_t)i*DIM, bnb_h+(size_t)i*DIM,
-          Wt + (size_t)(6+j)*DIM*DIM, Wt + (size_t)(12+j)*DIM*DIM,
-          Wt + (size_t)(i+1)*DIM*DIM, teb + (size_t)j*DIM, xbf, supbf, NN);
-    else
-      k_gemm_gate2<2><<<(NN+63)/64,256,0,stream>>>(hbf, stL,
-          bng_h+(size_t)i*DIM, bnb_h+(size_t)i*DIM,
-          Wt + (size_t)(6+j)*DIM*DIM, Wt + (size_t)(12+j)*DIM*DIM,
-          WtO, teb + (size_t)j*DIM, xbf, supO, NN);
-  }
-
-  k_spmm_out<<<NN/8,256,0,stream>>>(supO, sedge, offs, (float*)hbf, 6*NN, ostat8);
-  float* bufO = (float*)hbf;
-  k_reduce<<<512,256,0,stream>>>(bufO, ostat8, bng_o, bnb_o, verts, maskw, racc8, 98,
-                                 maskb, out, tick, 512);
-}
+  static int coopGrid = 0;
+  if (coopGrid == 0){
+    int maxb = 0;
+    hipOccupancyMaxActiveBlocksPerMultiprocessor(&maxb, (const void*)k_net, 256, 0);
+    if (maxb < 1) maxb = 1;
+    coopGrid = maxb * 256;
+    if (coopGrid > 2048) coopGrid = 2048;
+  }
+  KP p;
+  p.verts = verts; p.emb = emb; p.Wt = Wt; p.WtO = WtO;
+  p.sedge = sedge; p.offs = offs;
+  p.xbf = xbf; p.supbf = supbf; p.hbf = hbf; p.supO = supO;
+  p.stats = stats; p.ostat8 = ostat8; p.racc8 = racc8;
+  p.bng_h = bng_h; p.bnb_h = bnb_h; p.bng_o = bng_o; p.bnb_o = bnb_o;
+  p.teb = teb; p.maskw = maskw; p.maskb = maskb; p.out = out;
+  void* args[] = { &p };
+  hipLaunchCooperativeKernel((void*)k_net, dim3(coopGrid), dim3(256), args, 0, stream);
+}
```
